# Kernel tuning notes

Hardware: AMD Instinct MI355X
Metric: run time of the kernel (lower is better)

The kernel has to match this reference:

```python
import jax, jax.numpy as jnp
import numpy as np

N_NODES = 50000
NB = 32          # neighbor-list width per metapath
NFEAT = 128
NHID = 64
DIM_MP = 64
EDIM = 32
NMETA = 3
NCLASS = 8
B = 10000
ALPHA = 0.2


def setup_inputs() -> dict:
    key = jax.random.key(0)
    ks = jax.random.split(key, 16)
    s = 0.05
    return {
        "input": jax.random.normal(ks[0], (B, NFEAT), jnp.float32),
        "index": jax.random.randint(ks[1], (B,), 0, N_NODES),
        "node_emb": jax.random.normal(ks[2], (N_NODES, NFEAT), jnp.float32),
        "edge_index": jax.random.randint(ks[3], (NMETA, N_NODES, NB), 0, N_NODES, dtype=jnp.int32),
        "edge_emb": jax.random.normal(ks[4], (NMETA, N_NODES * NB, EDIM), jnp.float32) * 0.1,
        "n_sample": 32,
        "Wq1": jax.random.normal(ks[5], (NMETA, NFEAT, NHID), jnp.float32) * s,
        "Wk1": jax.random.normal(ks[6], (NMETA, NFEAT, NHID), jnp.float32) * s,
        "a1": jax.random.normal(ks[7], (NMETA, 2 * NHID + EDIM), jnp.float32) * s,
        "Wq2": jax.random.normal(ks[8], (NMETA, NHID, DIM_MP), jnp.float32) * s,
        "Wk2": jax.random.normal(ks[9], (NMETA, NFEAT, DIM_MP), jnp.float32) * s,
        "a2": jax.random.normal(ks[10], (NMETA, 2 * DIM_MP + EDIM), jnp.float32) * s,
        "a_mp": jax.random.normal(ks[11], (DIM_MP,), jnp.float32) * s,
        "Wc": jax.random.normal(ks[12], (DIM_MP, NCLASS), jnp.float32) * s,
        "bc": jnp.zeros((NCLASS,), jnp.float32),
    }


def _aggr(x, index, node_emb, nbr_tab, e_tab, Wq, Wk, a, out_dim, n_sample):
    """GAT-style edge-embedding attention aggregation over sampled neighbors.
    x:[B,in]  nbr_tab:[N,NB] int  e_tab:[N,NB,E]
    """
    nbrs = nbr_tab[index][:, :n_sample]              # [B,S] gathered neighbor ids
    e_emb = e_tab[index][:, :n_sample]               # [B,S,E] per-edge embeddings
    hq = x @ Wq                                      # [B,out]
    hk = node_emb[nbrs] @ Wk                         # [B,S,out] (irregular gather + GEMM)
    # attention score: a^T [hq || hk || e_ij]
    scores = (hq @ a[:out_dim])[:, None] + hk @ a[out_dim:2 * out_dim] + e_emb @ a[2 * out_dim:]
    scores = jax.nn.leaky_relu(scores, ALPHA)        # [B,S]
    att = jax.nn.softmax(scores, axis=1)
    agg = jnp.einsum('bs,bso->bo', att, hk)          # scatter-weighted aggregation
    return jax.nn.elu(agg)


def reference(input, index, node_emb, edge_index, edge_emb,
              Wq1, Wk1, a1, Wq2, Wk2, a2, a_mp, Wc, bc, n_sample):
    embs = []
    for m in range(NMETA):  # fixed small metapath loop (structurally distinct params)
        nbr_tab = edge_index[m]                              # [N,NB]
        e_tab = edge_emb[m].reshape(N_NODES, NB, EDIM)       # [N,NB,E]
        x1 = _aggr(input, index, node_emb, nbr_tab, e_tab, Wq1[m], Wk1[m], a1[m], NHID, n_sample)
        x2 = _aggr(x1, index, node_emb, nbr_tab, e_tab, Wq2[m], Wk2[m], a2[m], DIM_MP, n_sample)
        embs.append(x2)
    emb = jnp.stack(embs)                                    # [M,B,R]
    # metapath-level attention fusion
    e = jax.nn.leaky_relu(emb @ a_mp, ALPHA)                 # [M,B]
    att = jax.nn.softmax(e, axis=0)
    fused = jnp.einsum('mb,mbr->br', att, emb)               # [B,R]
    logits = jax.nn.relu(fused @ Wc + bc)                    # [B,nclass]
    return jax.nn.log_softmax(logits, axis=1)
```

## Files before the change

### kernel.cpp

```cpp
#include <hip/hip_runtime.h>
#include <hip/hip_bf16.h>
#include <cstddef>

#define NNODES 50000
#define NBW    32
#define NFEAT  128
#define NHID   64
#define EDIM   32
#define NMETA  3
#define NCLASS 8
#define BB     10000
#define SS     32

#define OFF_HKA   9600000
#define OFF_WQ1V  9900000
#define OFF_WQ2V  9900384
#define OFF_WBF   9900576

typedef __attribute__((ext_vector_type(8))) short bf16x8;
typedef __attribute__((ext_vector_type(4))) float f32x4;

static __device__ __forceinline__ unsigned short f2bf(float x) {
    unsigned u = __float_as_uint(x);
    return (unsigned short)((u + 0x7fffu + ((u >> 16) & 1u)) >> 16);
}
static __device__ __forceinline__ float bf2f(unsigned short h) {
    return __uint_as_float(((unsigned)h) << 16);
}

__global__ void prep_kernel(const float* __restrict__ Wq1, const float* __restrict__ a1,
                            const float* __restrict__ Wq2, const float* __restrict__ a2,
                            const float* __restrict__ Wk1, const float* __restrict__ Wk2,
                            float* __restrict__ wq1v, float* __restrict__ wq2v,
                            unsigned short* __restrict__ Bf)
{
    int blk = blockIdx.x, t = threadIdx.x;
    if (blk < 24) {
        int id = blk * 256 + t;
        int lane = id & 63;
        int t4 = (id >> 6) & 3;
        int kk = (id >> 8) & 3;
        int mat = id >> 10;
        const float* W = (mat < 3) ? (Wk1 + (size_t)mat * 8192)
                                   : (Wk2 + (size_t)(mat - 3) * 8192);
        int c  = t4 * 16 + (lane & 15);
        int kb = kk * 32 + (lane >> 4) * 8;
        unsigned short* dst = Bf + (size_t)id * 8;
        #pragma unroll
        for (int j = 0; j < 8; ++j) dst[j] = f2bf(W[(size_t)(kb + j) * 64 + c]);
    } else {
        int m = blk - 24;
        if (t < 128) {
            float acc = 0.f;
            const float* w = Wq1 + (m * 128 + t) * 64;
            const float* a = a1 + m * 160;
            #pragma unroll 8
            for (int c = 0; c < 64; ++c) acc += w[c] * a[c];
            wq1v[m * 128 + t] = acc;
        } else if (t < 192) {
            int f = t - 128;
            float acc = 0.f;
            const float* w = Wq2 + (m * 64 + f) * 64;
            const float* a = a2 + m * 160;
            #pragma unroll 8
            for (int c = 0; c < 64; ++c) acc += w[c] * a[c];
            wq2v[m * 64 + f] = acc;
        }
    }
}

__global__ __launch_bounds__(256) void hk_mfma6(const float* __restrict__ node_emb,
                                                const unsigned short* __restrict__ Bf,
                                                const float* __restrict__ a1,
                                                const float* __restrict__ a2,
                                                unsigned short* __restrict__ HKb,
                                                float* __restrict__ hka)
{
    __shared__ char lds_a[64 * 256];
    int nbase = blockIdx.x * 64;
    int t = threadIdx.x;

    #pragma unroll
    for (int i = 0; i < 8; ++i) {
        int fi = (i * 256 + t) * 4;
        int row = fi >> 7, k0 = fi & 127;
        int gn = nbase + row;
        float4 v = (gn < NNODES) ? *(const float4*)(node_emb + (size_t)gn * 128 + k0)
                                 : float4{0.f, 0.f, 0.f, 0.f};
        unsigned lo = (unsigned)f2bf(v.x) | ((unsigned)f2bf(v.y) << 16);
        unsigned hi = (unsigned)f2bf(v.z) | ((unsigned)f2bf(v.w) << 16);
        int byte = (row * 256 + k0 * 2) ^ ((row & 7) << 4);
        *(uint2*)(lds_a + byte) = uint2{lo, hi};
    }
    __syncthreads();

    int w = t >> 6, lane = t & 63;
    int row_l = lane & 15, kgrp = lane >> 4;
    int row = w * 16 + row_l;

    bf16x8 afr[4];
    #pragma unroll
    for (int kk = 0; kk < 4; ++kk) {
        int byte = (row * 256 + kk * 64 + kgrp * 16) ^ ((row_l & 7) << 4);
        afr[kk] = *(const bf16x8*)(lds_a + byte);
    }

    int col0 = lane & 15;
    #pragma unroll
    for (int mat = 0; mat < 6; ++mat) {
        const float* ak = ((mat >= 3) ? (a2 + (mat - 3) * 160) : (a1 + mat * 160)) + 64;
        f32x4 acc[4];
        #pragma unroll
        for (int j = 0; j < 4; ++j) acc[j] = f32x4{0.f, 0.f, 0.f, 0.f};
        #pragma unroll
        for (int kk = 0; kk < 4; ++kk) {
            #pragma unroll
            for (int t4 = 0; t4 < 4; ++t4) {
                bf16x8 b = *(const bf16x8*)(Bf + ((size_t)((mat * 4 + kk) * 4 + t4) * 64 + lane) * 8);
                acc[t4] = __builtin_amdgcn_mfma_f32_16x16x32_bf16(afr[kk], b, acc[t4], 0, 0, 0);
            }
        }
        float akv[4];
        #pragma unroll
        for (int t4 = 0; t4 < 4; ++t4) akv[t4] = ak[t4 * 16 + col0];
        #pragma unroll
        for (int r = 0; r < 4; ++r) {
            int n = nbase + w * 16 + kgrp * 4 + r;
            float hp = acc[0][r] * akv[0] + acc[1][r] * akv[1]
                     + acc[2][r] * akv[2] + acc[3][r] * akv[3];
            #pragma unroll
            for (int off = 8; off; off >>= 1) hp += __shfl_xor(hp, off, 16);
            if (n < NNODES) {
                unsigned short* dst = HKb + ((size_t)mat * NNODES + n) * 64;
                #pragma unroll
                for (int t4 = 0; t4 < 4; ++t4) dst[t4 * 16 + col0] = f2bf(acc[t4][r]);
                if (col0 == 0) hka[(size_t)mat * NNODES + n] = hp;
            }
        }
    }
}

__global__ __launch_bounds__(192) void fused_kernel(const float* __restrict__ input,
                                                    const int* __restrict__ index,
                                                    const int* __restrict__ edge_index,
                                                    const float* __restrict__ edge_emb,
                                                    const unsigned short* __restrict__ HKb,
                                                    const float* __restrict__ hka,
                                                    const float* __restrict__ wq1v,
                                                    const float* __restrict__ wq2v,
                                                    const float* __restrict__ a1,
                                                    const float* __restrict__ a2,
                                                    const float* __restrict__ a_mp,
                                                    const float* __restrict__ Wc,
                                                    const float* __restrict__ bc,
                                                    float* __restrict__ out)
{
    __shared__ float s_e[3][32][33];
    __shared__ float s_in[128];
    __shared__ int   s_nbr[3][32];
    __shared__ float s_att[3][32];
    __shared__ float s_ed1[3][32];
    __shared__ float s_emb[3][64];
    __shared__ float s_sc[3];

    int t = threadIdx.x, w = t >> 6, lane = t & 63;
    int m = w;
    int b = blockIdx.x;
    int idx = index[b];

    if (t < 128) s_in[t] = input[(size_t)b * 128 + t];

    const float4* src = (const float4*)(edge_emb + ((size_t)m * NNODES + idx) * (NBW * EDIM));
    float4 ef[4];
    #pragma unroll
    for (int i = 0; i < 4; ++i) ef[i] = src[i * 64 + lane];
    #pragma unroll
    for (int i = 0; i < 4; ++i) {
        int li = i * 64 + lane;
        int r = li >> 3, c4 = (li & 7) * 4;
        s_e[m][r][c4]     = ef[i].x;
        s_e[m][r][c4 + 1] = ef[i].y;
        s_e[m][r][c4 + 2] = ef[i].z;
        s_e[m][r][c4 + 3] = ef[i].w;
    }
    int nbr = 0;
    if (lane < 32) {
        nbr = edge_index[((size_t)m * NNODES + idx) * NBW + lane];
        s_nbr[m][lane] = nbr;
    }
    __syncthreads();

    int s = lane & 31, lvl = lane >> 5;
    const float* ae = (lvl ? a2 : a1) + m * 160 + 128;
    float ed = 0.f;
    #pragma unroll
    for (int k = 0; k < 32; ++k) ed += s_e[m][s][k] * ae[k];
    if (lvl) s_ed1[m][s] = ed;

    float hv = s_in[lane] * wq1v[m * 128 + lane] + s_in[lane + 64] * wq1v[m * 128 + lane + 64];
    #pragma unroll
    for (int off = 32; off; off >>= 1) hv += __shfl_xor(hv, off, 64);

    if (lane < 32) {
        float sc = hv + hka[(size_t)m * NNODES + nbr] + ed;
        sc = sc > 0.f ? sc : 0.2f * sc;
        float mx = sc;
        #pragma unroll
        for (int off = 16; off; off >>= 1) mx = fmaxf(mx, __shfl_xor(mx, off, 32));
        float p = expf(sc - mx);
        float sm = p;
        #pragma unroll
        for (int off = 16; off; off >>= 1) sm += __shfl_xor(sm, off, 32);
        s_att[m][lane] = p / sm;
    }
    __syncthreads();

    const unsigned short* tab1 = HKb + (size_t)m * NNODES * 64;
    float acc = 0.f;
    #pragma unroll
    for (int s2 = 0; s2 < 32; ++s2)
        acc += s_att[m][s2] * bf2f(tab1[(size_t)s_nbr[m][s2] * 64 + lane]);
    float x = acc > 0.f ? acc : expm1f(acc);

    float hv2 = x * wq2v[m * 64 + lane];
    #pragma unroll
    for (int off = 32; off; off >>= 1) hv2 += __shfl_xor(hv2, off, 64);

    if (lane < 32) {
        float sc = hv2 + hka[(size_t)(3 + m) * NNODES + nbr] + s_ed1[m][lane];
        sc = sc > 0.f ? sc : 0.2f * sc;
        float mx = sc;
        #pragma unroll
        for (int off = 16; off; off >>= 1) mx = fmaxf(mx, __shfl_xor(mx, off, 32));
        float p = expf(sc - mx);
        float sm = p;
        #pragma unroll
        for (int off = 16; off; off >>= 1) sm += __shfl_xor(sm, off, 32);
        s_att[m][lane] = p / sm;
    }
    __syncthreads();

    const unsigned short* tab2 = HKb + (size_t)(3 + m) * NNODES * 64;
    acc = 0.f;
    #pragma unroll
    for (int s2 = 0; s2 < 32; ++s2)
        acc += s_att[m][s2] * bf2f(tab2[(size_t)s_nbr[m][s2] * 64 + lane]);
    float emb_c = acc > 0.f ? acc : expm1f(acc);
    s_emb[m][lane] = emb_c;

    float ev = emb_c * a_mp[lane];
    #pragma unroll
    for (int off = 32; off; off >>= 1) ev += __shfl_xor(ev, off, 64);
    if (lane == 0) s_sc[m] = ev > 0.f ? ev : 0.2f * ev;
    __syncthreads();

    if (w == 0) {
        float e0 = s_sc[0], e1 = s_sc[1], e2 = s_sc[2];
        float mx = fmaxf(e0, fmaxf(e1, e2));
        float p0 = expf(e0 - mx), p1 = expf(e1 - mx), p2 = expf(e2 - mx);
        float sm = p0 + p1 + p2;
        float fused = (p0 * s_emb[0][lane] + p1 * s_emb[1][lane] + p2 * s_emb[2][lane]) / sm;

        float lg[NCLASS];
        #pragma unroll
        for (int j = 0; j < NCLASS; ++j) {
            float v = fused * Wc[lane * NCLASS + j];
            #pragma unroll
            for (int off = 32; off; off >>= 1) v += __shfl_xor(v, off, 64);
            lg[j] = fmaxf(v + bc[j], 0.f);
        }
        float m8 = lg[0];
        #pragma unroll
        for (int j = 1; j < NCLASS; ++j) m8 = fmaxf(m8, lg[j]);
        float se = 0.f;
        #pragma unroll
        for (int j = 0; j < NCLASS; ++j) se += expf(lg[j] - m8);
        float ls = logf(se);
        #pragma unroll
        for (int j = 0; j < NCLASS; ++j) {
            if (lane == j) out[(size_t)b * NCLASS + j] = lg[j] - m8 - ls;
        }
    }
}

extern "C" void kernel_launch(void* const* d_in, const int* in_sizes, int n_in,
                              void* d_out, int out_size, void* d_ws, size_t ws_size,
                              hipStream_t stream)
{
    const float* input     = (const float*)d_in[0];
    const int*   index     = (const int*)d_in[1];
    const float* node_emb  = (const float*)d_in[2];
    const int*   edge_index= (const int*)d_in[3];
    const float* edge_emb  = (const float*)d_in[4];
    const float* Wq1 = (const float*)d_in[6];
    const float* Wk1 = (const float*)d_in[7];
    const float* a1  = (const float*)d_in[8];
    const float* Wq2 = (const float*)d_in[9];
    const float* Wk2 = (const float*)d_in[10];
    const float* a2  = (const float*)d_in[11];
    const float* a_mp= (const float*)d_in[12];
    const float* Wc  = (const float*)d_in[13];
    const float* bc  = (const float*)d_in[14];

    float* ws = (float*)d_ws;
    unsigned short* HKb = (unsigned short*)d_ws;
    float* hka  = ws + OFF_HKA;
    float* wq1v = ws + OFF_WQ1V;
    float* wq2v = ws + OFF_WQ2V;
    unsigned short* Bf = (unsigned short*)(ws + OFF_WBF);

    prep_kernel<<<dim3(27), dim3(256), 0, stream>>>(Wq1, a1, Wq2, a2, Wk1, Wk2,
                                                    wq1v, wq2v, Bf);
    hk_mfma6<<<dim3((NNODES + 63) / 64), dim3(256), 0, stream>>>(
        node_emb, Bf, a1, a2, HKb, hka);
    fused_kernel<<<dim3(BB), dim3(192), 0, stream>>>(
        input, index, edge_index, edge_emb, HKb, hka, wq1v, wq2v,
        a1, a2, a_mp, Wc, bc, (float*)d_out);
}
```

Measured before the change: 95.71 us.

## Move edge-embedding dot products into the HK GEMM kernel and drop syncs

Adds a block range to the middle kernel that computes per-edge attention dot products (edge_emb · a) for both levels into a workspace buffer, so they run alongside the node GEMM. The fused kernel then reads 64 precomputed floats per metapath instead of loading 4KB of edge embeddings and doing the dot in LDS. The change also hoists the hka gathers before the first barrier and removes two __syncthreads, relying on each wave touching only its own s_att row. This trades an extra global write and read of the edge scores for a shorter critical path in the gather-heavy fused kernel.

```diff
diff --git a/kernel.cpp b/kernel.cpp
--- a/kernel.cpp
+++ b/kernel.cpp
@@ -16,6 +16,10 @@
 #define OFF_WQ1V  9900000
 #define OFF_WQ2V  9900384
 #define OFF_WBF   9900576
+#define OFF_EDOT  9925152
+
+#define NEDOTBLK  7500
+#define NGEMMBLK  782
 
 typedef __attribute__((ext_vector_type(8))) short bf16x8;
 typedef __attribute__((ext_vector_type(4))) float f32x4;
@@ -69,72 +73,105 @@
     }
 }
 
-__global__ __launch_bounds__(256) void hk_mfma6(const float* __restrict__ node_emb,
-                                                const unsigned short* __restrict__ Bf,
-                                                const float* __restrict__ a1,
-                                                const float* __restrict__ a2,
-                                                unsigned short* __restrict__ HKb,
-                                                float* __restrict__ hka)
+__global__ __launch_bounds__(256) void mid_kernel(const float* __restrict__ node_emb,
+                                                  const unsigned short* __restrict__ Bf,
+                                                  const float* __restrict__ a1,
+                                                  const float* __restrict__ a2,
+                                                  const int* __restrict__ index,
+                                                  const float* __restrict__ edge_emb,
+                                                  unsigned short* __restrict__ HKb,
+                                                  float* __restrict__ hka,
+                                                  float* __restrict__ edotw)
 {
-    __shared__ char lds_a[64 * 256];
-    int nbase = blockIdx.x * 64;
-    int t = threadIdx.x;
-
-    #pragma unroll
-    for (int i = 0; i < 8; ++i) {
-        int fi = (i * 256 + t) * 4;
-        int row = fi >> 7, k0 = fi & 127;
-        int gn = nbase + row;
-        float4 v = (gn < NNODES) ? *(const float4*)(node_emb + (size_t)gn * 128 + k0)
-                                 : float4{0.f, 0.f, 0.f, 0.f};
-        unsigned lo = (unsigned)f2bf(v.x) | ((unsigned)f2bf(v.y) << 16);
-        unsigned hi = (unsigned)f2bf(v.z) | ((unsigned)f2bf(v.w) << 16);
-        int byte = (row * 256 + k0 * 2) ^ ((row & 7) << 4);
-        *(uint2*)(lds_a + byte) = uint2{lo, hi};
-    }
-    __syncthreads();
-
-    int w = t >> 6, lane = t & 63;
-    int row_l = lane & 15, kgrp = lane >> 4;
-    int row = w * 16 + row_l;
-
-    bf16x8 afr[4];
-    #pragma unroll
-    for (int kk = 0; kk < 4; ++kk) {
-        int byte = (row * 256 + kk * 64 + kgrp * 16) ^ ((row_l & 7) << 4);
-        afr[kk] = *(const bf16x8*)(lds_a + byte);
-    }
-
-    int col0 = lane & 15;
-    #pragma unroll
-    for (int mat = 0; mat < 6; ++mat) {
-        const float* ak = ((mat >= 3) ? (a2 + (mat - 3) * 160) : (a1 + mat * 160)) + 64;
-        f32x4 acc[4];
-        #pragma unroll
-        for (int j = 0; j < 4; ++j) acc[j] = f32x4{0.f, 0.f, 0.f, 0.f};
+    __shared__ char lds[16896];
+    int bid = blockIdx.x, t = threadIdx.x;
+
+    if (bid < NEDOTBLK) {
+        float (*s_e)[32][33] = (float (*)[32][33])lds;
+        int w = t >> 6, lane = t & 63;
+        int m = bid / (BB / 4);
+        int b = (bid % (BB / 4)) * 4 + w;
+        int idx = index[b];
+        const float4* src = (const float4*)(edge_emb + ((size_t)m * NNODES + idx) * (NBW * EDIM));
+        float4 ef[4];
+        #pragma unroll
+        for (int i = 0; i < 4; ++i) ef[i] = src[i * 64 + lane];
+        #pragma unroll
+        for (int i = 0; i < 4; ++i) {
+            int li = i * 64 + lane;
+            int r = li >> 3, c4 = (li & 7) * 4;
+            s_e[w][r][c4]     = ef[i].x;
+            s_e[w][r][c4 + 1] = ef[i].y;
+            s_e[w][r][c4 + 2] = ef[i].z;
+            s_e[w][r][c4 + 3] = ef[i].w;
+        }
+        __syncthreads();
+        int s = lane & 31, lvl = lane >> 5;
+        const float* ae = (lvl ? a2 : a1) + m * 160 + 128;
+        float acc = 0.f;
+        #pragma unroll
+        for (int k = 0; k < 32; ++k) acc += s_e[w][s][k] * ae[k];
+        edotw[((size_t)m * BB + b) * 64 + lane] = acc;
+    } else {
+        char* lds_a = lds;
+        int nbase = (bid - NEDOTBLK) * 64;
+
+        #pragma unroll
+        for (int i = 0; i < 8; ++i) {
+            int fi = (i * 256 + t) * 4;
+            int row = fi >> 7, k0 = fi & 127;
+            int gn = nbase + row;
+            float4 v = (gn < NNODES) ? *(const float4*)(node_emb + (size_t)gn * 128 + k0)
+                                     : float4{0.f, 0.f, 0.f, 0.f};
+            unsigned lo = (unsigned)f2bf(v.x) | ((unsigned)f2bf(v.y) << 16);
+            unsigned hi = (unsigned)f2bf(v.z) | ((unsigned)f2bf(v.w) << 16);
+            int byte = (row * 256 + k0 * 2) ^ ((row & 7) << 4);
+            *(uint2*)(lds_a + byte) = uint2{lo, hi};
+        }
+        __syncthreads();
+
+        int w = t >> 6, lane = t & 63;
+        int row_l = lane & 15, kgrp = lane >> 4;
+        int row = w * 16 + row_l;
+
+        bf16x8 afr[4];
         #pragma unroll
         for (int kk = 0; kk < 4; ++kk) {
-            #pragma unroll
-            for (int t4 = 0; t4 < 4; ++t4) {
-                bf16x8 b = *(const bf16x8*)(Bf + ((size_t)((mat * 4 + kk) * 4 + t4) * 64 + lane) * 8);
-                acc[t4] = __builtin_amdgcn_mfma_f32_16x16x32_bf16(afr[kk], b, acc[t4], 0, 0, 0);
+            int byte = (row * 256 + kk * 64 + kgrp * 16) ^ ((row_l & 7) << 4);
+            afr[kk] = *(const bf16x8*)(lds_a + byte);
+        }
+
+        int col0 = lane & 15;
+        #pragma unroll
+        for (int mat = 0; mat < 6; ++mat) {
+            const float* ak = ((mat >= 3) ? (a2 + (mat - 3) * 160) : (a1 + mat * 160)) + 64;
+            f32x4 acc[4];
+            #pragma unroll
+            for (int j = 0; j < 4; ++j) acc[j] = f32x4{0.f, 0.f, 0.f, 0.f};
+            #pragma unroll
+            for (int kk = 0; kk < 4; ++kk) {
+                #pragma unroll
+                for (int t4 = 0; t4 < 4; ++t4) {
+                    bf16x8 b = *(const bf16x8*)(Bf + ((size_t)((mat * 4 + kk) * 4 + t4) * 64 + lane) * 8);
+                    acc[t4] = __builtin_amdgcn_mfma_f32_16x16x32_bf16(afr[kk], b, acc[t4], 0, 0, 0);
+                }
             }
-        }
-        float akv[4];
-        #pragma unroll
-        for (int t4 = 0; t4 < 4; ++t4) akv[t4] = ak[t4 * 16 + col0];
-        #pragma unroll
-        for (int r = 0; r < 4; ++r) {
-            int n = nbase + w * 16 + kgrp * 4 + r;
-            float hp = acc[0][r] * akv[0] + acc[1][r] * akv[1]
-                     + acc[2][r] * akv[2] + acc[3][r] * akv[3];
-            #pragma unroll
-            for (int off = 8; off; off >>= 1) hp += __shfl_xor(hp, off, 16);
-            if (n < NNODES) {
-                unsigned short* dst = HKb + ((size_t)mat * NNODES + n) * 64;
+            float akv[4];
+            #pragma unroll
+            for (int t4 = 0; t4 < 4; ++t4) akv[t4] = ak[t4 * 16 + col0];
+            #pragma unroll
+            for (int r = 0; r < 4; ++r) {
+                int n = nbase + w * 16 + kgrp * 4 + r;
+                float hp = acc[0][r] * akv[0] + acc[1][r] * akv[1]
+                         + acc[2][r] * akv[2] + acc[3][r] * akv[3];
                 #pragma unroll
-                for (int t4 = 0; t4 < 4; ++t4) dst[t4 * 16 + col0] = f2bf(acc[t4][r]);
-                if (col0 == 0) hka[(size_t)mat * NNODES + n] = hp;
+                for (int off = 8; off; off >>= 1) hp += __shfl_xor(hp, off, 16);
+                if (n < NNODES) {
+                    unsigned short* dst = HKb + ((size_t)mat * NNODES + n) * 64;
+                    #pragma unroll
+                    for (int t4 = 0; t4 < 4; ++t4) dst[t4 * 16 + col0] = f2bf(acc[t4][r]);
+                    if (col0 == 0) hka[(size_t)mat * NNODES + n] = hp;
+                }
             }
         }
     }
@@ -143,19 +180,16 @@
 __global__ __launch_bounds__(192) void fused_kernel(const float* __restrict__ input,
                                                     const int* __restrict__ index,
                                                     const int* __restrict__ edge_index,
-                                                    const float* __restrict__ edge_emb,
+                                                    const float* __restrict__ edotw,
                                                     const unsigned short* __restrict__ HKb,
                                                     const float* __restrict__ hka,
                                                     const float* __restrict__ wq1v,
                                                     const float* __restrict__ wq2v,
-                                                    const float* __restrict__ a1,
-                                                    const float* __restrict__ a2,
                                                     const float* __restrict__ a_mp,
                                                     const float* __restrict__ Wc,
                                                     const float* __restrict__ bc,
                                                     float* __restrict__ out)
 {
-    __shared__ float s_e[3][32][33];
     __shared__ float s_in[128];
     __shared__ int   s_nbr[3][32];
     __shared__ float s_att[3][32];
@@ -170,39 +204,25 @@
 
     if (t < 128) s_in[t] = input[(size_t)b * 128 + t];
 
-    const float4* src = (const float4*)(edge_emb + ((size_t)m * NNODES + idx) * (NBW * EDIM));
-    float4 ef[4];
-    #pragma unroll
-    for (int i = 0; i < 4; ++i) ef[i] = src[i * 64 + lane];
-    #pragma unroll
-    for (int i = 0; i < 4; ++i) {
-        int li = i * 64 + lane;
-        int r = li >> 3, c4 = (li & 7) * 4;
-        s_e[m][r][c4]     = ef[i].x;
-        s_e[m][r][c4 + 1] = ef[i].y;
-        s_e[m][r][c4 + 2] = ef[i].z;
-        s_e[m][r][c4 + 3] = ef[i].w;
-    }
+    float ed = edotw[((size_t)m * BB + b) * 64 + lane];
+    if (lane >= 32) s_ed1[m][lane - 32] = ed;
+
     int nbr = 0;
+    float hka1 = 0.f, hka2 = 0.f;
     if (lane < 32) {
         nbr = edge_index[((size_t)m * NNODES + idx) * NBW + lane];
         s_nbr[m][lane] = nbr;
+        hka1 = hka[(size_t)m * NNODES + nbr];
+        hka2 = hka[(size_t)(3 + m) * NNODES + nbr];
     }
     __syncthreads();
 
-    int s = lane & 31, lvl = lane >> 5;
-    const float* ae = (lvl ? a2 : a1) + m * 160 + 128;
-    float ed = 0.f;
-    #pragma unroll
-    for (int k = 0; k < 32; ++k) ed += s_e[m][s][k] * ae[k];
-    if (lvl) s_ed1[m][s] = ed;
-
     float hv = s_in[lane] * wq1v[m * 128 + lane] + s_in[lane + 64] * wq1v[m * 128 + lane + 64];
     #pragma unroll
     for (int off = 32; off; off >>= 1) hv += __shfl_xor(hv, off, 64);
 
     if (lane < 32) {
-        float sc = hv + hka[(size_t)m * NNODES + nbr] + ed;
+        float sc = hv + hka1 + ed;
         sc = sc > 0.f ? sc : 0.2f * sc;
         float mx = sc;
         #pragma unroll
@@ -213,7 +233,6 @@
         for (int off = 16; off; off >>= 1) sm += __shfl_xor(sm, off, 32);
         s_att[m][lane] = p / sm;
     }
-    __syncthreads();
 
     const unsigned short* tab1 = HKb + (size_t)m * NNODES * 64;
     float acc = 0.f;
@@ -227,7 +246,7 @@
     for (int off = 32; off; off >>= 1) hv2 += __shfl_xor(hv2, off, 64);
 
     if (lane < 32) {
-        float sc = hv2 + hka[(size_t)(3 + m) * NNODES + nbr] + s_ed1[m][lane];
+        float sc = hv2 + hka2 + s_ed1[m][lane];
         sc = sc > 0.f ? sc : 0.2f * sc;
         float mx = sc;
         #pragma unroll
@@ -238,7 +257,6 @@
         for (int off = 16; off; off >>= 1) sm += __shfl_xor(sm, off, 32);
         s_att[m][lane] = p / sm;
     }
-    __syncthreads();
 
     const unsigned short* tab2 = HKb + (size_t)(3 + m) * NNODES * 64;
     acc = 0.f;
@@ -308,12 +326,13 @@
     float* wq1v = ws + OFF_WQ1V;
     float* wq2v = ws + OFF_WQ2V;
     unsigned short* Bf = (unsigned short*)(ws + OFF_WBF);
+    float* edotw = ws + OFF_EDOT;
 
     prep_kernel<<<dim3(27), dim3(256), 0, stream>>>(Wq1, a1, Wq2, a2, Wk1, Wk2,
                                                     wq1v, wq2v, Bf);
-    hk_mfma6<<<dim3((NNODES + 63) / 64), dim3(256), 0, stream>>>(
-        node_emb, Bf, a1, a2, HKb, hka);
+    mid_kernel<<<dim3(NEDOTBLK + NGEMMBLK), dim3(256), 0, stream>>>(
+        node_emb, Bf, a1, a2, index, edge_emb, HKb, hka, edotw);
     fused_kernel<<<dim3(BB), dim3(192), 0, stream>>>(
-        input, index, edge_index, edge_emb, HKb, hka, wq1v, wq2v,
-        a1, a2, a_mp, Wc, bc, (float*)d_out);
-}
+        input, index, edge_index, edotw, HKb, hka, wq1v, wq2v,
+        a_mp, Wc, bc, (float*)d_out);
+}
```

New measurement: 101.0 us. +5.5%, slower.

## Interleave level-1/level-2 HK tables and replace LDS staging with shuffles

Applied to the files above, without the earlier changes.

The per-node projected key tables for both attention levels are interleaved so that one 32-bit gather per neighbor fetches both bf16 values, and the two hka scalars are paired into a float2. The fused kernel issues all 32 neighbor gathers up front into registers, before the first softmax, instead of doing two dependent gather passes. The shared-memory staging of edge embeddings, neighbors and attention weights, along with the block barriers, is replaced by wave shuffles. In exchange the code uses more registers, which may lower occupancy, and the GEMM epilogue now does strided 2-byte stores.

```diff
diff --git a/kernel.cpp b/kernel.cpp
--- a/kernel.cpp
+++ b/kernel.cpp
@@ -17,6 +17,8 @@
 #define OFF_WQ2V  9900384
 #define OFF_WBF   9900576
 
+#define NGEMMBLK  782
+
 typedef __attribute__((ext_vector_type(8))) short bf16x8;
 typedef __attribute__((ext_vector_type(4))) float f32x4;
 
@@ -26,6 +28,9 @@
 }
 static __device__ __forceinline__ float bf2f(unsigned short h) {
     return __uint_as_float(((unsigned)h) << 16);
+}
+static __device__ __forceinline__ float dot4(float4 a, float4 b) {
+    return a.x * b.x + a.y * b.y + a.z * b.z + a.w * b.w;
 }
 
 __global__ void prep_kernel(const float* __restrict__ Wq1, const float* __restrict__ a1,
@@ -73,8 +78,8 @@
                                                 const unsigned short* __restrict__ Bf,
                                                 const float* __restrict__ a1,
                                                 const float* __restrict__ a2,
-                                                unsigned short* __restrict__ HKb,
-                                                float* __restrict__ hka)
+                                                unsigned short* __restrict__ HKI,
+                                                float* __restrict__ hkaI)
 {
     __shared__ char lds_a[64 * 256];
     int nbase = blockIdx.x * 64;
@@ -108,7 +113,8 @@
     int col0 = lane & 15;
     #pragma unroll
     for (int mat = 0; mat < 6; ++mat) {
-        const float* ak = ((mat >= 3) ? (a2 + (mat - 3) * 160) : (a1 + mat * 160)) + 64;
+        int lvl = mat / 3, mm = mat % 3;
+        const float* ak = (lvl ? (a2 + mm * 160) : (a1 + mm * 160)) + 64;
         f32x4 acc[4];
         #pragma unroll
         for (int j = 0; j < 4; ++j) acc[j] = f32x4{0.f, 0.f, 0.f, 0.f};
@@ -131,10 +137,11 @@
             #pragma unroll
             for (int off = 8; off; off >>= 1) hp += __shfl_xor(hp, off, 16);
             if (n < NNODES) {
-                unsigned short* dst = HKb + ((size_t)mat * NNODES + n) * 64;
+                unsigned short* dst = HKI + (((size_t)mm * NNODES + n) * 64) * 2 + lvl;
                 #pragma unroll
-                for (int t4 = 0; t4 < 4; ++t4) dst[t4 * 16 + col0] = f2bf(acc[t4][r]);
-                if (col0 == 0) hka[(size_t)mat * NNODES + n] = hp;
+                for (int t4 = 0; t4 < 4; ++t4)
+                    dst[(t4 * 16 + col0) * 2] = f2bf(acc[t4][r]);
+                if (col0 == 0) hkaI[((size_t)mm * NNODES + n) * 2 + lvl] = hp;
             }
         }
     }
@@ -144,8 +151,8 @@
                                                     const int* __restrict__ index,
                                                     const int* __restrict__ edge_index,
                                                     const float* __restrict__ edge_emb,
-                                                    const unsigned short* __restrict__ HKb,
-                                                    const float* __restrict__ hka,
+                                                    const unsigned short* __restrict__ HKI,
+                                                    const float* __restrict__ hkaI,
                                                     const float* __restrict__ wq1v,
                                                     const float* __restrict__ wq2v,
                                                     const float* __restrict__ a1,
@@ -155,11 +162,6 @@
                                                     const float* __restrict__ bc,
                                                     float* __restrict__ out)
 {
-    __shared__ float s_e[3][32][33];
-    __shared__ float s_in[128];
-    __shared__ int   s_nbr[3][32];
-    __shared__ float s_att[3][32];
-    __shared__ float s_ed1[3][32];
     __shared__ float s_emb[3][64];
     __shared__ float s_sc[3];
 
@@ -168,41 +170,61 @@
     int b = blockIdx.x;
     int idx = index[b];
 
-    if (t < 128) s_in[t] = input[(size_t)b * 128 + t];
+    const int* eidx = edge_index + ((size_t)m * NNODES + idx) * NBW;
+    int nbr_l = eidx[lane & 31];
+
+    const unsigned short* TAB = HKI + (size_t)m * NNODES * 128;
+    unsigned h[32];
+    #pragma unroll
+    for (int j = 0; j < 32; ++j) {
+        const int rj = ((j & 3) << 3) | (j >> 2);
+        int nj = __shfl(nbr_l, rj, 64);
+        h[j] = *(const unsigned*)(TAB + (size_t)nj * 128 + lane * 2);
+    }
+
+    int rj_l = ((lane & 3) << 3) | ((lane >> 2) & 7);
+    int nbr_j = __shfl(nbr_l, rj_l, 64);
+    float2 ha = float2{0.f, 0.f};
+    if (lane < 32) ha = *(const float2*)(hkaI + ((size_t)m * NNODES + nbr_j) * 2);
 
     const float4* src = (const float4*)(edge_emb + ((size_t)m * NNODES + idx) * (NBW * EDIM));
     float4 ef[4];
     #pragma unroll
     for (int i = 0; i < 4; ++i) ef[i] = src[i * 64 + lane];
+
+    int k0 = (lane & 7) * 4;
+    float4 ae0 = *(const float4*)(a1 + m * 160 + 128 + k0);
+    float4 ae1 = *(const float4*)(a2 + m * 160 + 128 + k0);
+    float D0[4], D1[4];
     #pragma unroll
     for (int i = 0; i < 4; ++i) {
-        int li = i * 64 + lane;
-        int r = li >> 3, c4 = (li & 7) * 4;
-        s_e[m][r][c4]     = ef[i].x;
-        s_e[m][r][c4 + 1] = ef[i].y;
-        s_e[m][r][c4 + 2] = ef[i].z;
-        s_e[m][r][c4 + 3] = ef[i].w;
-    }
-    int nbr = 0;
-    if (lane < 32) {
-        nbr = edge_index[((size_t)m * NNODES + idx) * NBW + lane];
-        s_nbr[m][lane] = nbr;
-    }
-    __syncthreads();
-
-    int s = lane & 31, lvl = lane >> 5;
-    const float* ae = (lvl ? a2 : a1) + m * 160 + 128;
-    float ed = 0.f;
-    #pragma unroll
-    for (int k = 0; k < 32; ++k) ed += s_e[m][s][k] * ae[k];
-    if (lvl) s_ed1[m][s] = ed;
-
-    float hv = s_in[lane] * wq1v[m * 128 + lane] + s_in[lane + 64] * wq1v[m * 128 + lane + 64];
+        float p0 = dot4(ef[i], ae0), p1 = dot4(ef[i], ae1);
+        #pragma unroll
+        for (int off = 4; off; off >>= 1) {
+            p0 += __shfl_xor(p0, off, 64);
+            p1 += __shfl_xor(p1, off, 64);
+        }
+        D0[i] = p0; D1[i] = p1;
+    }
+    float t0[4], t1[4];
+    #pragma unroll
+    for (int i = 0; i < 4; ++i) {
+        int srcl = (lane >> 2) << 3;
+        t0[i] = __shfl(D0[i], srcl, 64);
+        t1[i] = __shfl(D1[i], srcl, 64);
+    }
+    int i_sel = lane & 3;
+    float ed0 = i_sel == 0 ? t0[0] : i_sel == 1 ? t0[1] : i_sel == 2 ? t0[2] : t0[3];
+    float ed1 = i_sel == 0 ? t1[0] : i_sel == 1 ? t1[1] : i_sel == 2 ? t1[2] : t1[3];
+
+    float hv = input[(size_t)b * 128 + lane] * wq1v[m * 128 + lane]
+             + input[(size_t)b * 128 + 64 + lane] * wq1v[m * 128 + 64 + lane];
     #pragma unroll
     for (int off = 32; off; off >>= 1) hv += __shfl_xor(hv, off, 64);
 
-    if (lane < 32) {
-        float sc = hv + hka[(size_t)m * NNODES + nbr] + ed;
+    float att_l = 0.f;
+    {
+        float sc = hv + ha.x + ed0;
         sc = sc > 0.f ? sc : 0.2f * sc;
         float mx = sc;
         #pragma unroll
@@ -211,23 +233,22 @@
         float sm = p;
         #pragma unroll
         for (int off = 16; off; off >>= 1) sm += __shfl_xor(sm, off, 32);
-        s_att[m][lane] = p / sm;
-    }
-    __syncthreads();
-
-    const unsigned short* tab1 = HKb + (size_t)m * NNODES * 64;
+        att_l = p / sm;
+    }
+
     float acc = 0.f;
     #pragma unroll
-    for (int s2 = 0; s2 < 32; ++s2)
-        acc += s_att[m][s2] * bf2f(tab1[(size_t)s_nbr[m][s2] * 64 + lane]);
+    for (int j = 0; j < 32; ++j)
+        acc += __shfl(att_l, j, 64) * bf2f((unsigned short)(h[j] & 0xffffu));
     float x = acc > 0.f ? acc : expm1f(acc);
 
     float hv2 = x * wq2v[m * 64 + lane];
     #pragma unroll
     for (int off = 32; off; off >>= 1) hv2 += __shfl_xor(hv2, off, 64);
 
-    if (lane < 32) {
-        float sc = hv2 + hka[(size_t)(3 + m) * NNODES + nbr] + s_ed1[m][lane];
+    float att2_l = 0.f;
+    {
+        float sc = hv2 + ha.y + ed1;
         sc = sc > 0.f ? sc : 0.2f * sc;
         float mx = sc;
         #pragma unroll
@@ -236,15 +257,13 @@
         float sm = p;
         #pragma unroll
         for (int off = 16; off; off >>= 1) sm += __shfl_xor(sm, off, 32);
-        s_att[m][lane] = p / sm;
-    }
-    __syncthreads();
-
-    const unsigned short* tab2 = HKb + (size_t)(3 + m) * NNODES * 64;
+        att2_l = p / sm;
+    }
+
     acc = 0.f;
     #pragma unroll
-    for (int s2 = 0; s2 < 32; ++s2)
-        acc += s_att[m][s2] * bf2f(tab2[(size_t)s_nbr[m][s2] * 64 + lane]);
+    for (int j = 0; j < 32; ++j)
+        acc += __shfl(att2_l, j, 64) * bf2f((unsigned short)(h[j] >> 16));
     float emb_c = acc > 0.f ? acc : expm1f(acc);
     s_emb[m][lane] = emb_c;
 
@@ -303,17 +322,17 @@
     const float* bc  = (const float*)d_in[14];
 
     float* ws = (float*)d_ws;
-    unsigned short* HKb = (unsigned short*)d_ws;
-    float* hka  = ws + OFF_HKA;
+    unsigned short* HKI = (unsigned short*)d_ws;
+    float* hkaI = ws + OFF_HKA;
     float* wq1v = ws + OFF_WQ1V;
     float* wq2v = ws + OFF_WQ2V;
     unsigned short* Bf = (unsigned short*)(ws + OFF_WBF);
 
     prep_kernel<<<dim3(27), dim3(256), 0, stream>>>(Wq1, a1, Wq2, a2, Wk1, Wk2,
                                                     wq1v, wq2v, Bf);
-    hk_mfma6<<<dim3((NNODES + 63) / 64), dim3(256), 0, stream>>>(
-        node_emb, Bf, a1, a2, HKb, hka);
+    hk_mfma6<<<dim3(NGEMMBLK), dim3(256), 0, stream>>>(
+        node_emb, Bf, a1, a2, HKI, hkaI);
     fused_kernel<<<dim3(BB), dim3(192), 0, stream>>>(
-        input, index, edge_index, edge_emb, HKb, hka, wq1v, wq2v,
+        input, index, edge_index, edge_emb, HKI, hkaI, wq1v, wq2v,
         a1, a2, a_mp, Wc, bc, (float*)d_out);
 }
```

After: 114.2 us. 1.19x slower.

## Interleave both attention levels' neighbor tables so one gather serves both

Applied to the files above, without the earlier changes.

The projection kernel now computes the level-1 and level-2 key tables together for each metapath. It packs the two bf16 values into one 32-bit word per element and stores both attention-bias scalars as a float2. The fused kernel gathers each neighbor row once, up front, into 32 registers, overlapping it with the edge-embedding load, and reuses those registers for both aggregation levels. Because each metapath lives entirely inside one wavefront, the block-wide barriers between the score and aggregation phases are removed. The cost is higher register pressure from the held gather results, plus reliance on wavefront-local ordering of shared-memory writes and reads without explicit barriers.

```diff
diff --git a/kernel.cpp b/kernel.cpp
--- a/kernel.cpp
+++ b/kernel.cpp
@@ -16,6 +16,8 @@
 #define OFF_WQ1V  9900000
 #define OFF_WQ2V  9900384
 #define OFF_WBF   9900576
+
+#define NGEMMBLK  782
 
 typedef __attribute__((ext_vector_type(8))) short bf16x8;
 typedef __attribute__((ext_vector_type(4))) float f32x4;
@@ -73,8 +75,8 @@
                                                 const unsigned short* __restrict__ Bf,
                                                 const float* __restrict__ a1,
                                                 const float* __restrict__ a2,
-                                                unsigned short* __restrict__ HKb,
-                                                float* __restrict__ hka)
+                                                unsigned* __restrict__ HKI,
+                                                float* __restrict__ hkaI)
 {
     __shared__ char lds_a[64 * 256];
     int nbase = blockIdx.x * 64;
@@ -107,34 +109,45 @@
 
     int col0 = lane & 15;
     #pragma unroll
-    for (int mat = 0; mat < 6; ++mat) {
-        const float* ak = ((mat >= 3) ? (a2 + (mat - 3) * 160) : (a1 + mat * 160)) + 64;
-        f32x4 acc[4];
-        #pragma unroll
-        for (int j = 0; j < 4; ++j) acc[j] = f32x4{0.f, 0.f, 0.f, 0.f};
+    for (int mm = 0; mm < 3; ++mm) {
+        f32x4 acc0[4], acc1[4];
+        #pragma unroll
+        for (int j = 0; j < 4; ++j) { acc0[j] = f32x4{0,0,0,0}; acc1[j] = f32x4{0,0,0,0}; }
         #pragma unroll
         for (int kk = 0; kk < 4; ++kk) {
             #pragma unroll
             for (int t4 = 0; t4 < 4; ++t4) {
-                bf16x8 b = *(const bf16x8*)(Bf + ((size_t)((mat * 4 + kk) * 4 + t4) * 64 + lane) * 8);
-                acc[t4] = __builtin_amdgcn_mfma_f32_16x16x32_bf16(afr[kk], b, acc[t4], 0, 0, 0);
+                bf16x8 b0 = *(const bf16x8*)(Bf + ((size_t)((mm * 4 + kk) * 4 + t4) * 64 + lane) * 8);
+                bf16x8 b1 = *(const bf16x8*)(Bf + ((size_t)(((3 + mm) * 4 + kk) * 4 + t4) * 64 + lane) * 8);
+                acc0[t4] = __builtin_amdgcn_mfma_f32_16x16x32_bf16(afr[kk], b0, acc0[t4], 0, 0, 0);
+                acc1[t4] = __builtin_amdgcn_mfma_f32_16x16x32_bf16(afr[kk], b1, acc1[t4], 0, 0, 0);
             }
         }
-        float akv[4];
-        #pragma unroll
-        for (int t4 = 0; t4 < 4; ++t4) akv[t4] = ak[t4 * 16 + col0];
+        const float* ak0 = a1 + mm * 160 + 64;
+        const float* ak1 = a2 + mm * 160 + 64;
+        float akv0[4], akv1[4];
+        #pragma unroll
+        for (int t4 = 0; t4 < 4; ++t4) { akv0[t4] = ak0[t4 * 16 + col0]; akv1[t4] = ak1[t4 * 16 + col0]; }
         #pragma unroll
         for (int r = 0; r < 4; ++r) {
             int n = nbase + w * 16 + kgrp * 4 + r;
-            float hp = acc[0][r] * akv[0] + acc[1][r] * akv[1]
-                     + acc[2][r] * akv[2] + acc[3][r] * akv[3];
+            float hp0 = acc0[0][r] * akv0[0] + acc0[1][r] * akv0[1]
+                      + acc0[2][r] * akv0[2] + acc0[3][r] * akv0[3];
+            float hp1 = acc1[0][r] * akv1[0] + acc1[1][r] * akv1[1]
+                      + acc1[2][r] * akv1[2] + acc1[3][r] * akv1[3];
             #pragma unroll
-            for (int off = 8; off; off >>= 1) hp += __shfl_xor(hp, off, 16);
+            for (int off = 8; off; off >>= 1) {
+                hp0 += __shfl_xor(hp0, off, 16);
+                hp1 += __shfl_xor(hp1, off, 16);
+            }
             if (n < NNODES) {
-                unsigned short* dst = HKb + ((size_t)mat * NNODES + n) * 64;
+                unsigned* dst = HKI + ((size_t)mm * NNODES + n) * 64;
                 #pragma unroll
-                for (int t4 = 0; t4 < 4; ++t4) dst[t4 * 16 + col0] = f2bf(acc[t4][r]);
-                if (col0 == 0) hka[(size_t)mat * NNODES + n] = hp;
+                for (int t4 = 0; t4 < 4; ++t4)
+                    dst[t4 * 16 + col0] = (unsigned)f2bf(acc0[t4][r])
+                                        | ((unsigned)f2bf(acc1[t4][r]) << 16);
+                if (col0 == 0)
+                    *(float2*)(hkaI + ((size_t)mm * NNODES + n) * 2) = float2{hp0, hp1};
             }
         }
     }
@@ -144,8 +157,8 @@
                                                     const int* __restrict__ index,
                                                     const int* __restrict__ edge_index,
                                                     const float* __restrict__ edge_emb,
-                                                    const unsigned short* __restrict__ HKb,
-                                                    const float* __restrict__ hka,
+                                                    const unsigned* __restrict__ HKI,
+                                                    const float* __restrict__ hkaI,
                                                     const float* __restrict__ wq1v,
                                                     const float* __restrict__ wq2v,
                                                     const float* __restrict__ a1,
@@ -156,7 +169,6 @@
                                                     float* __restrict__ out)
 {
     __shared__ float s_e[3][32][33];
-    __shared__ float s_in[128];
     __shared__ int   s_nbr[3][32];
     __shared__ float s_att[3][32];
     __shared__ float s_ed1[3][32];
@@ -168,12 +180,23 @@
     int b = blockIdx.x;
     int idx = index[b];
 
-    if (t < 128) s_in[t] = input[(size_t)b * 128 + t];
+    const int* eidx = edge_index + ((size_t)m * NNODES + idx) * NBW;
+    int nbr_l = eidx[lane & 31];
+    if (lane < 32) s_nbr[m][lane] = nbr_l;
+
+    float2 ha = *(const float2*)(hkaI + ((size_t)m * NNODES + nbr_l) * 2);
 
     const float4* src = (const float4*)(edge_emb + ((size_t)m * NNODES + idx) * (NBW * EDIM));
     float4 ef[4];
     #pragma unroll
     for (int i = 0; i < 4; ++i) ef[i] = src[i * 64 + lane];
+
+    const unsigned* TAB = HKI + (size_t)m * NNODES * 64;
+    unsigned h[32];
+    #pragma unroll
+    for (int j = 0; j < 32; ++j)
+        h[j] = TAB[(size_t)s_nbr[m][j] * 64 + lane];
+
     #pragma unroll
     for (int i = 0; i < 4; ++i) {
         int li = i * 64 + lane;
@@ -183,12 +206,6 @@
         s_e[m][r][c4 + 2] = ef[i].z;
         s_e[m][r][c4 + 3] = ef[i].w;
     }
-    int nbr = 0;
-    if (lane < 32) {
-        nbr = edge_index[((size_t)m * NNODES + idx) * NBW + lane];
-        s_nbr[m][lane] = nbr;
-    }
-    __syncthreads();
 
     int s = lane & 31, lvl = lane >> 5;
     const float* ae = (lvl ? a2 : a1) + m * 160 + 128;
@@ -197,12 +214,13 @@
     for (int k = 0; k < 32; ++k) ed += s_e[m][s][k] * ae[k];
     if (lvl) s_ed1[m][s] = ed;
 
-    float hv = s_in[lane] * wq1v[m * 128 + lane] + s_in[lane + 64] * wq1v[m * 128 + lane + 64];
+    float hv = input[(size_t)b * 128 + lane] * wq1v[m * 128 + lane]
+             + input[(size_t)b * 128 + 64 + lane] * wq1v[m * 128 + 64 + lane];
     #pragma unroll
     for (int off = 32; off; off >>= 1) hv += __shfl_xor(hv, off, 64);
 
     if (lane < 32) {
-        float sc = hv + hka[(size_t)m * NNODES + nbr] + ed;
+        float sc = hv + ha.x + ed;
         sc = sc > 0.f ? sc : 0.2f * sc;
         float mx = sc;
         #pragma unroll
@@ -213,13 +231,11 @@
         for (int off = 16; off; off >>= 1) sm += __shfl_xor(sm, off, 32);
         s_att[m][lane] = p / sm;
     }
-    __syncthreads();
-
-    const unsigned short* tab1 = HKb + (size_t)m * NNODES * 64;
+
     float acc = 0.f;
     #pragma unroll
-    for (int s2 = 0; s2 < 32; ++s2)
-        acc += s_att[m][s2] * bf2f(tab1[(size_t)s_nbr[m][s2] * 64 + lane]);
+    for (int j = 0; j < 32; ++j)
+        acc += s_att[m][j] * bf2f((unsigned short)(h[j] & 0xffffu));
     float x = acc > 0.f ? acc : expm1f(acc);
 
     float hv2 = x * wq2v[m * 64 + lane];
@@ -227,7 +243,7 @@
     for (int off = 32; off; off >>= 1) hv2 += __shfl_xor(hv2, off, 64);
 
     if (lane < 32) {
-        float sc = hv2 + hka[(size_t)(3 + m) * NNODES + nbr] + s_ed1[m][lane];
+        float sc = hv2 + ha.y + s_ed1[m][lane];
         sc = sc > 0.f ? sc : 0.2f * sc;
         float mx = sc;
         #pragma unroll
@@ -238,13 +254,11 @@
         for (int off = 16; off; off >>= 1) sm += __shfl_xor(sm, off, 32);
         s_att[m][lane] = p / sm;
     }
-    __syncthreads();
-
-    const unsigned short* tab2 = HKb + (size_t)(3 + m) * NNODES * 64;
+
     acc = 0.f;
     #pragma unroll
-    for (int s2 = 0; s2 < 32; ++s2)
-        acc += s_att[m][s2] * bf2f(tab2[(size_t)s_nbr[m][s2] * 64 + lane]);
+    for (int j = 0; j < 32; ++j)
+        acc += s_att[m][j] * bf2f((unsigned short)(h[j] >> 16));
     float emb_c = acc > 0.f ? acc : expm1f(acc);
     s_emb[m][lane] = emb_c;
 
@@ -303,17 +317,17 @@
     const float* bc  = (const float*)d_in[14];
 
     float* ws = (float*)d_ws;
-    unsigned short* HKb = (unsigned short*)d_ws;
-    float* hka  = ws + OFF_HKA;
+    unsigned* HKI = (unsigned*)d_ws;
+    float* hkaI = ws + OFF_HKA;
     float* wq1v = ws + OFF_WQ1V;
     float* wq2v = ws + OFF_WQ2V;
     unsigned short* Bf = (unsigned short*)(ws + OFF_WBF);
 
     prep_kernel<<<dim3(27), dim3(256), 0, stream>>>(Wq1, a1, Wq2, a2, Wk1, Wk2,
                                                     wq1v, wq2v, Bf);
-    hk_mfma6<<<dim3((NNODES + 63) / 64), dim3(256), 0, stream>>>(
-        node_emb, Bf, a1, a2, HKb, hka);
+    hk_mfma6<<<dim3(NGEMMBLK), dim3(256), 0, stream>>>(
+        node_emb, Bf, a1, a2, HKI, hkaI);
     fused_kernel<<<dim3(BB), dim3(192), 0, stream>>>(
-        input, index, edge_index, edge_emb, HKb, hka, wq1v, wq2v,
+        input, index, edge_index, edge_emb, HKI, hkaI, wq1v, wq2v,
         a1, a2, a_mp, Wc, bc, (float*)d_out);
 }
```

Result: no change. 94.97 us (-0.8%).
